# Kernel tuning notes

Measured on AMD Instinct MI355X. Metric: run time of the kernel, lower is better.

Reference implementation:

```python
import jax, jax.numpy as jnp
from jax import lax
import numpy as np

N = 16384      # points
NIN = 64       # input feature dim
NOUT = 128     # output feature dim
RATIO = 0.25
R = 0.5        # ball-query radius
K = 64         # max neighbors
M = int(N * RATIO)  # sampled centroids (ceil not needed: exact)
DIM = NIN + 3  # PointConv MLP input dim
EPS = 1e-5     # BatchNorm eps (eval mode, running_mean=0, running_var=1)


def _fps(pos, m):
    """Farthest point sampling (deterministic start at index 0)."""
    p = lax.stop_gradient(pos)
    def step(carry, _):
        dmin, last = carry
        dist = jnp.sum((p - p[last]) ** 2, axis=-1)
        dmin = jnp.minimum(dmin, dist)
        return (dmin, jnp.argmax(dmin).astype(jnp.int32)), last
    init = (jnp.full((p.shape[0],), jnp.inf, p.dtype), jnp.int32(0))
    _, idx = lax.scan(step, init, None, length=m)
    return idx  # [m]


def _bn_eval(h, g, b):
    # eval-mode BatchNorm1d with running_mean=0, running_var=1
    return g * (h * np.float32(1.0 / np.sqrt(1.0 + EPS))) + b


def setup_inputs() -> dict:
    key = jax.random.key(0)
    ks = jax.random.split(key, 8)
    x = jax.random.normal(ks[0], (N, NIN), jnp.float32)
    pos = jax.random.normal(ks[1], (N, 3), jnp.float32)
    batch = jnp.zeros((N,), jnp.int32)  # single point cloud
    def lin(k, i, o):
        return jax.random.normal(k, (i, o), jnp.float32) * np.float32(1.0 / np.sqrt(i))
    w1 = lin(ks[2], DIM, DIM)
    b1 = jnp.zeros((DIM,), jnp.float32)
    g1 = 1.0 + 0.1 * jax.random.normal(ks[3], (DIM,), jnp.float32)
    be1 = 0.1 * jax.random.normal(ks[4], (DIM,), jnp.float32)
    w2 = lin(ks[5], DIM, NOUT)
    b2 = jnp.zeros((NOUT,), jnp.float32)
    g2 = 1.0 + 0.1 * jax.random.normal(ks[6], (NOUT,), jnp.float32)
    be2 = 0.1 * jax.random.normal(ks[7], (NOUT,), jnp.float32)
    return dict(x=x, pos=pos, batch=batch, w1=w1, b1=b1, g1=g1, be1=be1,
                w2=w2, b2=b2, g2=g2, be2=be2)


def reference(x, pos, batch, w1, b1, g1, be1, w2, b2, g2, be2):
    # 1) FPS sampling
    idx = _fps(pos, M)                      # [M]
    pos_s = pos[idx]                        # [M,3]
    # 2) radius (ball) query: K nearest within radius R, mask the rest
    d2 = jnp.sum((lax.stop_gradient(pos_s)[:, None, :] -
                  lax.stop_gradient(pos)[None, :, :]) ** 2, axis=-1)  # [M,N]
    neg = jnp.where(d2 <= R * R, -d2, -jnp.inf)
    vals, nbr = lax.top_k(neg, K)           # [M,K]
    valid = vals > -jnp.inf                 # each centroid contains itself -> >=1 valid
    safe = jnp.where(valid, nbr, 0)
    # 3) PointConv message: MLP([x_j, pos_j - pos_i]) then max-aggregate
    x_j = x[safe]                           # [M,K,NIN]
    rel = pos[safe] - pos_s[:, None, :]     # [M,K,3]
    h = jnp.concatenate([x_j, rel], axis=-1)            # [M,K,DIM]
    h = _bn_eval(jax.nn.relu(h @ w1 + b1), g1, be1)
    h = _bn_eval(jax.nn.relu(h @ w2 + b2), g2, be2)      # [M,K,NOUT]
    msg = jnp.where(valid[..., None], h, -jnp.inf)
    x_out = jnp.max(msg, axis=1)            # [M,NOUT]
    return (x_out, pos_s, batch[idx], idx)
```

## Files before the change

kernel.cpp:

```cpp
#include <hip/hip_runtime.h>
#include <hip/hip_bf16.h>

#define N_PTS 16384
#define M_CTR 4096
#define NIN   64
#define NOUT  128
#define DIM   67
#define KNBR  64
#define R2    0.25f
#define BNI   0.9999950000374997f


__device__ inline unsigned long long shfl_xor_u64(unsigned long long v, int m){
  int lo = __shfl_xor((int)(unsigned)v, m, 64);
  int hi = __shfl_xor((int)(unsigned)(v >> 32), m, 64);
  return ((unsigned long long)(unsigned)hi << 32) | (unsigned)lo;
}

#define FPS_T 1024
#define FPS_K (N_PTS / FPS_T)
#define FPS_W (FPS_T / 64)

__global__ __launch_bounds__(FPS_T) void fps_kernel(const float* __restrict__ pos,
                                                    int* __restrict__ sel) {
  __shared__ unsigned long long wkey[2][FPS_W];
  const int t = threadIdx.x;
  float px[FPS_K], py[FPS_K], pz[FPS_K], dmin[FPS_K];
#pragma unroll
  for (int k = 0; k < FPS_K; k++) {
    int g = t + FPS_T * k;
    px[k] = pos[3*g+0]; py[k] = pos[3*g+1]; pz[k] = pos[3*g+2];
    dmin[k] = 3.4028235e38f;
  }
  if (t == 0) sel[0] = 0;
  float X = pos[0], Y = pos[1], Z = pos[2];
  for (int s = 1; s < M_CTR; s++) {
    float v = 0.0f;
    int iL = 0;
#pragma unroll
    for (int k = 0; k < FPS_K; k++) {
      float dx = __fsub_rn(px[k], X);
      float dy = __fsub_rn(py[k], Y);
      float dz = __fsub_rn(pz[k], Z);
      float q  = __fadd_rn(__fadd_rn(__fmul_rn(dx,dx), __fmul_rn(dy,dy)), __fmul_rn(dz,dz));
      float d  = fminf(dmin[k], q);
      dmin[k]  = d;
      bool c = d > v;
      v  = c ? d : v;
      iL = c ? k : iL;
    }
    unsigned g = (unsigned)t + ((unsigned)iL * FPS_T);
    unsigned long long key =
        (((unsigned long long)__float_as_uint(v)) << 32) |
        (unsigned long long)(0xFFFFFFFFu - g);
#pragma unroll
    for (int m = 32; m >= 1; m >>= 1) {
      unsigned long long o = shfl_xor_u64(key, m);
      key = (o > key) ? o : key;
    }
    if ((t & 63) == 0) wkey[s & 1][t >> 6] = key;
    __syncthreads();
    unsigned long long kb = wkey[s & 1][0];
#pragma unroll
    for (int w = 1; w < FPS_W; w++) {
      unsigned long long o = wkey[s & 1][w];
      kb = (o > kb) ? o : kb;
    }
    unsigned gw = 0xFFFFFFFFu - (unsigned)(kb & 0xFFFFFFFFull);
    if (t == 0) sel[s] = (int)gw;
    X = pos[3*gw+0]; Y = pos[3*gw+1]; Z = pos[3*gw+2];
  }
}

__global__ __launch_bounds__(64) void xw1_kernel(const float* __restrict__ x,
                                                 const float* __restrict__ w1,
                                                 float* __restrict__ U) {
  __shared__ float xs[NIN];
  const int n = blockIdx.x, t = threadIdx.x;
  xs[t] = x[n * NIN + t];
  __syncthreads();
  for (int c = t; c < DIM; c += 64) {
    float acc = 0.0f;
#pragma unroll 8
    for (int r = 0; r < NIN; r++) acc = fmaf(xs[r], w1[r * DIM + c], acc);
    U[n * DIM + c] = acc;
  }
}

#define CAP 2048
__global__ __launch_bounds__(64) void ballq_kernel(const float* __restrict__ pos,
                                                   const int* __restrict__ sel,
                                                   int* __restrict__ nbr,
                                                   int* __restrict__ nvalid) {
  __shared__ unsigned long long keys[CAP];
  __shared__ int cnt;
  const int i = blockIdx.x;
  const int lane = threadIdx.x;
  if (lane == 0) cnt = 0;
  __syncthreads();
  int ci = sel[i]; ci = min(max(ci, 0), N_PTS - 1);
  const float X = pos[3*ci], Y = pos[3*ci+1], Z = pos[3*ci+2];
  for (int k = 0; k < N_PTS / 64; k++) {
    int g = lane + 64 * k;
    float dx = __fsub_rn(pos[3*g+0], X);
    float dy = __fsub_rn(pos[3*g+1], Y);
    float dz = __fsub_rn(pos[3*g+2], Z);
    float q  = __fadd_rn(__fadd_rn(__fmul_rn(dx,dx), __fmul_rn(dy,dy)), __fmul_rn(dz,dz));
    if (q <= R2) {
      int p = atomicAdd(&cnt, 1);
      if (p < CAP)
        keys[p] = (((unsigned long long)__float_as_uint(q)) << 32) | (unsigned)g;
    }
  }
  __syncthreads();
  const int n = min(cnt, CAP);
  for (int r = 0; r < KNBR; r++) {
    unsigned long long mk = ~0ull; int mp = -1;
    for (int p = lane; p < n; p += 64) {
      unsigned long long kk = keys[p];
      if (kk < mk) { mk = kk; mp = p; }
    }
    unsigned long long rk = mk;
#pragma unroll
    for (int m = 32; m >= 1; m >>= 1) {
      unsigned long long o = shfl_xor_u64(rk, m);
      rk = (o < rk) ? o : rk;
    }
    if (rk != ~0ull && rk == mk && mp >= 0) keys[mp] = ~0ull;
    if (lane == 0)
      nbr[i * KNBR + r] = (rk != ~0ull) ? (int)(unsigned)(rk & 0xFFFFFFFFull) : 0;
  }
  if (lane == 0) nvalid[i] = min(n, KNBR);
}

__global__ __launch_bounds__(128) void mlp_u_kernel(
    const float* __restrict__ U, const float* __restrict__ pos,
    const float* __restrict__ w1, const float* __restrict__ b1,
    const float* __restrict__ g1, const float* __restrict__ be1,
    const float* __restrict__ w2, const float* __restrict__ b2,
    const float* __restrict__ g2, const float* __restrict__ be2,
    const int* __restrict__ sel, const int* __restrict__ nbr,
    const int* __restrict__ nvalid, float* __restrict__ out) {
  __shared__ float Us[KNBR * DIM];
  __shared__ float relx[KNBR], rely[KNBR], relz[KNBR];
  __shared__ float h1[DIM];
  __shared__ float w1r[3][DIM], b1s[DIM], g1s[DIM], be1s[DIM];
  __shared__ int nbrs_s[KNBR];
  const int i = blockIdx.x, t = threadIdx.x;
  int nv = nvalid[i]; nv = min(max(nv, 0), KNBR);
  float w2r[DIM];
#pragma unroll
  for (int c = 0; c < DIM; c++) w2r[c] = w2[c * NOUT + t];
  if (t < KNBR) {
    int nj = (t < nv) ? nbr[i * KNBR + t] : 0;
    nbrs_s[t] = min(max(nj, 0), N_PTS - 1);
  }
  if (t < DIM) {
    w1r[0][t] = w1[64*DIM + t]; w1r[1][t] = w1[65*DIM + t]; w1r[2][t] = w1[66*DIM + t];
    b1s[t] = b1[t]; g1s[t] = g1[t]; be1s[t] = be1[t];
  }
  __syncthreads();
  int ci = sel[i]; ci = min(max(ci, 0), N_PTS - 1);
  const float cx = pos[3*ci], cy = pos[3*ci+1], cz = pos[3*ci+2];
  if (t < KNBR && t < nv) {
    int nj = nbrs_s[t];
    relx[t] = pos[3*nj+0] - cx; rely[t] = pos[3*nj+1] - cy; relz[t] = pos[3*nj+2] - cz;
  }
  for (int e = t; e < nv * DIM; e += 128) {
    int r = e / DIM, c = e - r * DIM;
    Us[e] = U[nbrs_s[r] * DIM + c];
  }
  __syncthreads();
  const float b2d = b2[t], g2d = g2[t], be2d = be2[t];
  float omax = -3.4028235e38f;
  for (int j = 0; j < nv; j++) {
    if (t < DIM) {
      float z = Us[j*DIM + t];
      z = fmaf(relx[j], w1r[0][t], z);
      z = fmaf(rely[j], w1r[1][t], z);
      z = fmaf(relz[j], w1r[2][t], z);
      z += b1s[t];
      z = fmaxf(z, 0.0f);
      h1[t] = g1s[t] * (z * BNI) + be1s[t];
    }
    __syncthreads();
    float a0 = 0.f, a1 = 0.f, a2 = 0.f, a3 = 0.f;
#pragma unroll
    for (int c = 0; c < 64; c += 4) {
      a0 = fmaf(h1[c+0], w2r[c+0], a0);
      a1 = fmaf(h1[c+1], w2r[c+1], a1);
      a2 = fmaf(h1[c+2], w2r[c+2], a2);
      a3 = fmaf(h1[c+3], w2r[c+3], a3);
    }
    a0 = fmaf(h1[64], w2r[64], a0);
    a1 = fmaf(h1[65], w2r[65], a1);
    a2 = fmaf(h1[66], w2r[66], a2);
    float acc = ((a0 + a1) + (a2 + a3)) + b2d;
    float h2v = g2d * (fmaxf(acc, 0.0f) * BNI) + be2d;
    omax = fmaxf(omax, h2v);
    __syncthreads();
  }
  if (nv == 0) omax = 0.0f;
  out[i*NOUT + t] = omax;
}

__global__ __launch_bounds__(128) void mlp_direct_kernel(
    const float* __restrict__ x, const float* __restrict__ pos,
    const float* __restrict__ w1, const float* __restrict__ b1,
    const float* __restrict__ g1, const float* __restrict__ be1,
    const float* __restrict__ w2, const float* __restrict__ b2,
    const float* __restrict__ g2, const float* __restrict__ be2,
    const int* __restrict__ sel, const int* __restrict__ nbr,
    const int* __restrict__ nvalid, float* __restrict__ out) {
  __shared__ float xs[NIN];
  __shared__ float h1[DIM];
  __shared__ float rel[3];
  const int i = blockIdx.x, t = threadIdx.x;
  int ci = sel[i]; ci = min(max(ci, 0), N_PTS - 1);
  const float cx = pos[3*ci], cy = pos[3*ci+1], cz = pos[3*ci+2];
  int nv = nvalid[i]; nv = min(max(nv, 0), KNBR);
  float omax = -3.4028235e38f;
  for (int j = 0; j < nv; j++) {
    int nj = nbr[i*KNBR + j]; nj = min(max(nj, 0), N_PTS - 1);
    if (t < NIN) xs[t] = x[nj*NIN + t];
    if (t == 0) { rel[0] = pos[3*nj]-cx; rel[1] = pos[3*nj+1]-cy; rel[2] = pos[3*nj+2]-cz; }
    __syncthreads();
    if (t < DIM) {
      float z = b1[t];
      for (int r = 0; r < NIN; r++) z = fmaf(xs[r], w1[r*DIM + t], z);
      z = fmaf(rel[0], w1[64*DIM + t], z);
      z = fmaf(rel[1], w1[65*DIM + t], z);
      z = fmaf(rel[2], w1[66*DIM + t], z);
      z = fmaxf(z, 0.0f);
      h1[t] = g1[t] * (z * BNI) + be1[t];
    }
    __syncthreads();
    float acc = b2[t];
    for (int c = 0; c < DIM; c++) acc = fmaf(h1[c], w2[c*NOUT + t], acc);
    float h2v = g2[t] * (fmaxf(acc, 0.0f) * BNI) + be2[t];
    omax = fmaxf(omax, h2v);
    __syncthreads();
  }
  if (nv == 0) omax = 0.0f;
  out[i*NOUT + t] = omax;
}

__global__ void fin_kernel(const float* __restrict__ pos, const int* __restrict__ batch,
                           const int* __restrict__ sel, float* __restrict__ out) {
  int i = blockIdx.x * blockDim.x + threadIdx.x;
  if (i < M_CTR) {
    int s = sel[i];
    int sc = min(max(s, 0), N_PTS - 1);
    out[M_CTR*NOUT + 3*i + 0] = pos[3*sc+0];
    out[M_CTR*NOUT + 3*i + 1] = pos[3*sc+1];
    out[M_CTR*NOUT + 3*i + 2] = pos[3*sc+2];
    out[M_CTR*NOUT + 3*M_CTR + i] = (float)batch[sc];
    out[M_CTR*NOUT + 4*M_CTR + i] = (float)s;
  }
}

extern "C" void kernel_launch(void* const* d_in, const int* in_sizes, int n_in,
                              void* d_out, int out_size, void* d_ws, size_t ws_size,
                              hipStream_t stream) {
  const float* x   = (const float*)d_in[0];
  const float* pos = (const float*)d_in[1];
  const int*  batch= (const int*)d_in[2];
  const float* w1  = (const float*)d_in[3];
  const float* b1  = (const float*)d_in[4];
  const float* g1  = (const float*)d_in[5];
  const float* be1 = (const float*)d_in[6];
  const float* w2  = (const float*)d_in[7];
  const float* b2  = (const float*)d_in[8];
  const float* g2  = (const float*)d_in[9];
  const float* be2 = (const float*)d_in[10];
  float* out = (float*)d_out;

  char*  ws   = (char*)d_ws;
  int*   sel  = (int*)(ws);
  int*   nvld = (int*)(ws + 16384);
  int*   nbr  = (int*)(ws + 32768);
  float* U    = (float*)(ws + 1081344);
  const bool useU = (ws_size >= (size_t)1081344 + (size_t)N_PTS * DIM * 4);

  hipLaunchKernelGGL(fps_kernel,   dim3(1),      dim3(FPS_T), 0, stream, pos, sel);
  hipLaunchKernelGGL(ballq_kernel, dim3(M_CTR),  dim3(64),    0, stream, pos, sel, nbr, nvld);
  if (useU) {
    hipLaunchKernelGGL(xw1_kernel, dim3(N_PTS),  dim3(64),    0, stream, x, w1, U);
    hipLaunchKernelGGL(mlp_u_kernel, dim3(M_CTR), dim3(128),  0, stream,
                       U, pos, w1, b1, g1, be1, w2, b2, g2, be2, sel, nbr, nvld, out);
  } else {
    hipLaunchKernelGGL(mlp_direct_kernel, dim3(M_CTR), dim3(128), 0, stream,
                       x, pos, w1, b1, g1, be1, w2, b2, g2, be2, sel, nbr, nvld, out);
  }
  hipLaunchKernelGGL(fin_kernel,   dim3(16),     dim3(256),   0, stream, pos, batch, sel, out);
}
```

Before: 7.532 ms.

## Use packed FP32 math and tree reductions in FPS inner loop

Rewrites the per-thread FPS distance update to use v_pk_add/v_pk_mul on pairs of points, and replaces the serial argmax chain with a tree of fmaxf followed by an index search for the first matching value. The cross-wave reduction now reads shared memory as 128-bit vectors and combines them in a tree. The aim is to cut the VALU instruction count and dependency-chain latency in the serial 4096-step FPS loop, which dominates runtime. Negating X and adding it, instead of subtracting, keeps rounding identical. Tie-breaking still selects the lowest index.

```diff
diff --git a/kernel.cpp b/kernel.cpp
--- a/kernel.cpp
+++ b/kernel.cpp
@@ -11,44 +11,70 @@
 #define BNI   0.9999950000374997f
 
 
+typedef float v2f __attribute__((ext_vector_type(2)));
+
+static __device__ inline v2f pk_add(v2f a, v2f b) {
+  v2f d; asm("v_pk_add_f32 %0, %1, %2" : "=v"(d) : "v"(a), "v"(b)); return d;
+}
+static __device__ inline v2f pk_mul(v2f a, v2f b) {
+  v2f d; asm("v_pk_mul_f32 %0, %1, %2" : "=v"(d) : "v"(a), "v"(b)); return d;
+}
+
 __device__ inline unsigned long long shfl_xor_u64(unsigned long long v, int m){
   int lo = __shfl_xor((int)(unsigned)v, m, 64);
   int hi = __shfl_xor((int)(unsigned)(v >> 32), m, 64);
   return ((unsigned long long)(unsigned)hi << 32) | (unsigned)lo;
 }
+__device__ inline unsigned long long u64max(unsigned long long a, unsigned long long b){
+  return a > b ? a : b;
+}
 
 #define FPS_T 1024
 #define FPS_K (N_PTS / FPS_T)
+#define FPS_K2 (FPS_K / 2)
 #define FPS_W (FPS_T / 64)
 
-__global__ __launch_bounds__(FPS_T) void fps_kernel(const float* __restrict__ pos,
-                                                    int* __restrict__ sel) {
-  __shared__ unsigned long long wkey[2][FPS_W];
+__global__ __launch_bounds__(FPS_T, 4) void fps_kernel(const float* __restrict__ pos,
+                                                       int* __restrict__ sel) {
+  __shared__ __align__(16) unsigned long long wkey[2][FPS_W];
   const int t = threadIdx.x;
-  float px[FPS_K], py[FPS_K], pz[FPS_K], dmin[FPS_K];
-#pragma unroll
-  for (int k = 0; k < FPS_K; k++) {
-    int g = t + FPS_T * k;
-    px[k] = pos[3*g+0]; py[k] = pos[3*g+1]; pz[k] = pos[3*g+2];
-    dmin[k] = 3.4028235e38f;
+  v2f px[FPS_K2], py[FPS_K2], pz[FPS_K2];
+  float dmin[FPS_K];
+#pragma unroll
+  for (int j = 0; j < FPS_K2; j++) {
+    int g0 = t + FPS_T * (2*j);
+    int g1 = t + FPS_T * (2*j + 1);
+    px[j] = (v2f){pos[3*g0+0], pos[3*g1+0]};
+    py[j] = (v2f){pos[3*g0+1], pos[3*g1+1]};
+    pz[j] = (v2f){pos[3*g0+2], pos[3*g1+2]};
+    dmin[2*j] = 3.4028235e38f; dmin[2*j+1] = 3.4028235e38f;
   }
   if (t == 0) sel[0] = 0;
   float X = pos[0], Y = pos[1], Z = pos[2];
   for (int s = 1; s < M_CTR; s++) {
-    float v = 0.0f;
+    const float nX = -X, nY = -Y, nZ = -Z;
+    const v2f nXX = (v2f){nX, nX}, nYY = (v2f){nY, nY}, nZZ = (v2f){nZ, nZ};
+#pragma unroll
+    for (int j = 0; j < FPS_K2; j++) {
+      v2f dx = pk_add(px[j], nXX);
+      v2f dy = pk_add(py[j], nYY);
+      v2f dz = pk_add(pz[j], nZZ);
+      v2f xx = pk_mul(dx, dx);
+      v2f yy = pk_mul(dy, dy);
+      v2f zz = pk_mul(dz, dz);
+      v2f ss = pk_add(xx, yy);
+      v2f qq = pk_add(ss, zz);
+      dmin[2*j]   = fminf(dmin[2*j],   qq.x);
+      dmin[2*j+1] = fminf(dmin[2*j+1], qq.y);
+    }
+    float m0 = fmaxf(fmaxf(dmin[0], dmin[1]), fmaxf(dmin[2], dmin[3]));
+    float m1 = fmaxf(fmaxf(dmin[4], dmin[5]), fmaxf(dmin[6], dmin[7]));
+    float m2 = fmaxf(fmaxf(dmin[8], dmin[9]), fmaxf(dmin[10], dmin[11]));
+    float m3 = fmaxf(fmaxf(dmin[12], dmin[13]), fmaxf(dmin[14], dmin[15]));
+    float v = fmaxf(fmaxf(m0, m1), fmaxf(m2, m3));
     int iL = 0;
 #pragma unroll
-    for (int k = 0; k < FPS_K; k++) {
-      float dx = __fsub_rn(px[k], X);
-      float dy = __fsub_rn(py[k], Y);
-      float dz = __fsub_rn(pz[k], Z);
-      float q  = __fadd_rn(__fadd_rn(__fmul_rn(dx,dx), __fmul_rn(dy,dy)), __fmul_rn(dz,dz));
-      float d  = fminf(dmin[k], q);
-      dmin[k]  = d;
-      bool c = d > v;
-      v  = c ? d : v;
-      iL = c ? k : iL;
-    }
+    for (int k = FPS_K - 1; k >= 0; k--) iL = (dmin[k] == v) ? k : iL;
     unsigned g = (unsigned)t + ((unsigned)iL * FPS_T);
     unsigned long long key =
         (((unsigned long long)__float_as_uint(v)) << 32) |
@@ -60,12 +86,14 @@
     }
     if ((t & 63) == 0) wkey[s & 1][t >> 6] = key;
     __syncthreads();
-    unsigned long long kb = wkey[s & 1][0];
-#pragma unroll
-    for (int w = 1; w < FPS_W; w++) {
-      unsigned long long o = wkey[s & 1][w];
-      kb = (o > kb) ? o : kb;
-    }
+    const ulonglong2* wk2 = (const ulonglong2*)&wkey[s & 1][0];
+    ulonglong2 p0 = wk2[0], p1 = wk2[1], p2 = wk2[2], p3 = wk2[3];
+    ulonglong2 p4 = wk2[4], p5 = wk2[5], p6 = wk2[6], p7 = wk2[7];
+    unsigned long long a0 = u64max(u64max(p0.x, p0.y), u64max(p1.x, p1.y));
+    unsigned long long a1 = u64max(u64max(p2.x, p2.y), u64max(p3.x, p3.y));
+    unsigned long long a2 = u64max(u64max(p4.x, p4.y), u64max(p5.x, p5.y));
+    unsigned long long a3 = u64max(u64max(p6.x, p6.y), u64max(p7.x, p7.y));
+    unsigned long long kb = u64max(u64max(a0, a1), u64max(a2, a3));
     unsigned gw = 0xFFFFFFFFu - (unsigned)(kb & 0xFFFFFFFFull);
     if (t == 0) sel[s] = (int)gw;
     X = pos[3*gw+0]; Y = pos[3*gw+1]; Z = pos[3*gw+2];
```

Result: slower. 9.124 ms (+21.1%).

## Restructure FPS argmax reduction with tree max, ds_swizzle, and vectorized LDS reads

Applied to the files above, without the earlier changes.

Each FPS step now first finds the per-thread maximum with a tree of fmaxf, then recovers its index with a separate equality scan. The wave reduction becomes two 32-bit passes instead of 64-bit shuffles: a float max over ds_swizzle and one shfl, then a min over the candidate indices. The cross-wave reduction reads LDS as 128-bit ulonglong2 loads and combines them in a tree. The aim is to shorten the serial dependency chain and cut shuffle cost in the 4095-step sequential loop. It keeps lowest-index tie-breaking, but the code is harder to read.

```diff
diff --git a/kernel.cpp b/kernel.cpp
--- a/kernel.cpp
+++ b/kernel.cpp
@@ -16,14 +16,25 @@
   int hi = __shfl_xor((int)(unsigned)(v >> 32), m, 64);
   return ((unsigned long long)(unsigned)hi << 32) | (unsigned)lo;
 }
+__device__ inline unsigned long long u64max(unsigned long long a, unsigned long long b){
+  return a > b ? a : b;
+}
+template<int PAT>
+__device__ inline float swz_xor_f(float x){
+  return __int_as_float(__builtin_amdgcn_ds_swizzle(__float_as_int(x), PAT));
+}
+template<int PAT>
+__device__ inline unsigned swz_xor_u(unsigned x){
+  return (unsigned)__builtin_amdgcn_ds_swizzle((int)x, PAT);
+}
 
 #define FPS_T 1024
 #define FPS_K (N_PTS / FPS_T)
 #define FPS_W (FPS_T / 64)
 
-__global__ __launch_bounds__(FPS_T) void fps_kernel(const float* __restrict__ pos,
-                                                    int* __restrict__ sel) {
-  __shared__ unsigned long long wkey[2][FPS_W];
+__global__ __launch_bounds__(FPS_T, 4) void fps_kernel(const float* __restrict__ pos,
+                                                       int* __restrict__ sel) {
+  __shared__ __align__(16) unsigned long long wkey[2][FPS_W];
   const int t = threadIdx.x;
   float px[FPS_K], py[FPS_K], pz[FPS_K], dmin[FPS_K];
 #pragma unroll
@@ -35,37 +46,49 @@
   if (t == 0) sel[0] = 0;
   float X = pos[0], Y = pos[1], Z = pos[2];
   for (int s = 1; s < M_CTR; s++) {
-    float v = 0.0f;
-    int iL = 0;
 #pragma unroll
     for (int k = 0; k < FPS_K; k++) {
       float dx = __fsub_rn(px[k], X);
       float dy = __fsub_rn(py[k], Y);
       float dz = __fsub_rn(pz[k], Z);
       float q  = __fadd_rn(__fadd_rn(__fmul_rn(dx,dx), __fmul_rn(dy,dy)), __fmul_rn(dz,dz));
-      float d  = fminf(dmin[k], q);
-      dmin[k]  = d;
-      bool c = d > v;
-      v  = c ? d : v;
-      iL = c ? k : iL;
-    }
-    unsigned g = (unsigned)t + ((unsigned)iL * FPS_T);
-    unsigned long long key =
-        (((unsigned long long)__float_as_uint(v)) << 32) |
-        (unsigned long long)(0xFFFFFFFFu - g);
-#pragma unroll
-    for (int m = 32; m >= 1; m >>= 1) {
-      unsigned long long o = shfl_xor_u64(key, m);
-      key = (o > key) ? o : key;
-    }
-    if ((t & 63) == 0) wkey[s & 1][t >> 6] = key;
-    __syncthreads();
-    unsigned long long kb = wkey[s & 1][0];
-#pragma unroll
-    for (int w = 1; w < FPS_W; w++) {
-      unsigned long long o = wkey[s & 1][w];
-      kb = (o > kb) ? o : kb;
-    }
+      dmin[k]  = fminf(dmin[k], q);
+    }
+    float m0 = fmaxf(fmaxf(dmin[0],  dmin[1]),  fmaxf(dmin[2],  dmin[3]));
+    float m1 = fmaxf(fmaxf(dmin[4],  dmin[5]),  fmaxf(dmin[6],  dmin[7]));
+    float m2 = fmaxf(fmaxf(dmin[8],  dmin[9]),  fmaxf(dmin[10], dmin[11]));
+    float m3 = fmaxf(fmaxf(dmin[12], dmin[13]), fmaxf(dmin[14], dmin[15]));
+    float v  = fmaxf(fmaxf(m0, m1), fmaxf(m2, m3));
+    int iL = 0;
+#pragma unroll
+    for (int k = FPS_K - 1; k >= 0; k--) iL = (dmin[k] == v) ? k : iL;
+    unsigned g = (unsigned)t + ((unsigned)iL << 10);
+    float wv = v;
+    wv = fmaxf(wv, swz_xor_f<0x041F>(wv));
+    wv = fmaxf(wv, swz_xor_f<0x081F>(wv));
+    wv = fmaxf(wv, swz_xor_f<0x101F>(wv));
+    wv = fmaxf(wv, swz_xor_f<0x201F>(wv));
+    wv = fmaxf(wv, swz_xor_f<0x401F>(wv));
+    wv = fmaxf(wv, __int_as_float(__shfl_xor(__float_as_int(wv), 32, 64)));
+    unsigned c = (v == wv) ? g : 0xFFFFFFFFu;
+    c = min(c, swz_xor_u<0x041F>(c));
+    c = min(c, swz_xor_u<0x081F>(c));
+    c = min(c, swz_xor_u<0x101F>(c));
+    c = min(c, swz_xor_u<0x201F>(c));
+    c = min(c, swz_xor_u<0x401F>(c));
+    c = min(c, (unsigned)__shfl_xor((int)c, 32, 64));
+    if ((t & 63) == 0)
+      wkey[s & 1][t >> 6] = (((unsigned long long)__float_as_uint(wv)) << 32) |
+                            (unsigned long long)(0xFFFFFFFFu - c);
+    __syncthreads();
+    const ulonglong2* wk2 = (const ulonglong2*)&wkey[s & 1][0];
+    ulonglong2 p0 = wk2[0], p1 = wk2[1], p2 = wk2[2], p3 = wk2[3];
+    ulonglong2 p4 = wk2[4], p5 = wk2[5], p6 = wk2[6], p7 = wk2[7];
+    unsigned long long a0 = u64max(u64max(p0.x, p0.y), u64max(p1.x, p1.y));
+    unsigned long long a1 = u64max(u64max(p2.x, p2.y), u64max(p3.x, p3.y));
+    unsigned long long a2 = u64max(u64max(p4.x, p4.y), u64max(p5.x, p5.y));
+    unsigned long long a3 = u64max(u64max(p6.x, p6.y), u64max(p7.x, p7.y));
+    unsigned long long kb = u64max(u64max(a0, a1), u64max(a2, a3));
     unsigned gw = 0xFFFFFFFFu - (unsigned)(kb & 0xFFFFFFFFull);
     if (t == 0) sel[s] = (int)gw;
     X = pos[3*gw+0]; Y = pos[3*gw+1]; Z = pos[3*gw+2];
```

Measured after the change: 8.098 ms. +7.5%, slower.
